# Kernel tuning notes

Hardware: AMD Instinct MI355X
Metric: run time of the kernel (lower is better)

## Reference

```python
import jax, jax.numpy as jnp
import numpy as np

N, E, DIN, DOUT, H = 100000, 1600000, 128, 128, 4
DH = DOUT // H
EPS = 1e-9


def setup_inputs() -> dict:
    key = jax.random.key(0)
    ks = jax.random.split(key, 16)
    g = lambda k, shape, fan: (jax.random.uniform(k, shape, jnp.float32, -1.0, 1.0)
                               * np.sqrt(6.0 / fan)).astype(jnp.float32)
    return {
        "vecs": jax.random.normal(ks[0], (N, DIN), jnp.float32),
        "adj_vals": jax.random.uniform(ks[1], (E,), jnp.float32),
        "W0": g(ks[2], (DIN, DOUT), DIN + DOUT),
        "b0": jnp.zeros((DOUT,), jnp.float32),
        "W1": g(ks[3], (H, DIN, DH), DIN + DH),          # per-head order1 weights
        "b1": jnp.zeros((H, DH), jnp.float32),
        "att0": g(ks[4], (H, DH), 1 + DH),               # attention_0_h{k}
        "att1": g(ks[5], (H, DH), 1 + DH),               # attention_1_h{k}
        "att_b0": jnp.zeros((H,), jnp.float32),
        "att_b1": jnp.zeros((H,), jnp.float32),
        "off0": jnp.zeros((1, DOUT), jnp.float32),
        "sc0": jnp.ones((1, DOUT), jnp.float32),
        "off1": jnp.zeros((1, DOUT), jnp.float32),
        "sc1": jnp.ones((1, DOUT), jnp.float32),
        "adj_rows": jax.random.randint(ks[6], (E,), 0, N, jnp.int32),
        "adj_cols": jax.random.randint(ks[7], (E,), 0, N, jnp.int32),
    }


def _row_norm(x, offset, scale):
    # tf.nn.moments over axis=1 + batch_normalization (per-row "norm" bias)
    mean = jnp.mean(x, axis=1, keepdims=True)
    var = jnp.mean(jnp.square(x - mean), axis=1, keepdims=True)
    return scale * (x - mean) * jax.lax.rsqrt(var + EPS) + offset


def reference(vecs, adj_vals, W0, b0, W1, b1, att0, att1, att_b0, att_b1,
              off0, sc0, off1, sc1, adj_rows, adj_cols):
    # ----- order-0 (self) path -----
    ret_self = jax.nn.relu(vecs @ W0 + b0)                      # [N, DOUT]
    ret_self = _row_norm(ret_self, off0, sc0)

    # ----- order-1 (neighbor) path, all heads at once -----
    vw = jnp.einsum('nd,hdk->hnk', vecs, W1)                    # [H, N, DH]
    a_self = jnp.einsum('hnk,hk->hn', vw, att0) + att_b0[:, None]   # [H, N]
    a_neigh = jnp.einsum('hnk,hk->hn', vw, att1) + att_b1[:, None]  # [H, N]

    # per-edge attention: relu(a1[col] + a2[row]); reweight sparse adj values
    alpha = jax.nn.relu(a_neigh[:, adj_cols] + a_self[:, adj_rows])  # [H, E]
    w = adj_vals[None, :] * alpha                                    # [H, E]

    # sparse-dense matmul: scatter-add weighted neighbor features to rows
    msg = w[:, :, None] * vw[:, adj_cols, :]                         # [H, E, DH]
    agg = jax.vmap(lambda m: jax.ops.segment_sum(m, adj_rows, num_segments=N))(msg)  # [H, N, DH]

    # subgraph (training) path: act(spmm) + bias (bias OUTSIDE the relu)
    ret_neigh = jax.nn.relu(agg) + b1[:, None, :]                    # [H, N, DH]
    ret_neigh = jnp.transpose(ret_neigh, (1, 0, 2)).reshape(N, DOUT)  # concat heads
    ret_neigh = _row_norm(ret_neigh, off1, sc1)

    # aggr == 'mean'
    return ret_neigh + ret_self
```

## Files before the change

kernel.cpp:

```cpp
#include <hip/hip_runtime.h>

#define N_NODES 100000
#define N_EDGES 1600000
#define DIN 128
#define DOUT 128
#define NH 4
#define DH 32
#define EPS 1e-9f

#define NBUK 256
#define NBUK_USED 196
#define CBLK 784
#define EPB  2048
#define COLMASK 0x1FFFF

typedef short bf16x8 __attribute__((ext_vector_type(8)));
typedef float f32x4 __attribute__((ext_vector_type(4)));

__device__ inline unsigned short f2bf(float x) {
    unsigned u = __float_as_uint(x);
    unsigned r = (u + 0x7fffu + ((u >> 16) & 1u)) >> 16;
    return (unsigned short)r;
}
__device__ inline float bflo(unsigned v) { return __uint_as_float(v << 16); }
__device__ inline float bfhi(unsigned v) { return __uint_as_float(v & 0xffff0000u); }

__global__ void k_cast(const float* __restrict__ in, unsigned short* __restrict__ out) {
    int t = blockIdx.x * 256 + threadIdx.x;
    const float4* p = (const float4*)(in + (size_t)t * 8);
    float4 a = p[0], b = p[1];
    unsigned short o[8] = {f2bf(a.x), f2bf(a.y), f2bf(a.z), f2bf(a.w),
                           f2bf(b.x), f2bf(b.y), f2bf(b.z), f2bf(b.w)};
    *(bf16x8*)(out + (size_t)t * 8) = *(bf16x8*)o;
}

__global__ void k_build_wtb(const float* __restrict__ W0, const float* __restrict__ W1,
                            unsigned short* __restrict__ Wtb) {
    int idx = blockIdx.x * 256 + threadIdx.x;
    int j = idx >> 7;
    int k = idx & 127;
    float v;
    if (j < 128) v = W0[k * 128 + j];
    else {
        int f = j - 128;
        v = W1[(f >> 5) * (DIN * DH) + k * DH + (f & 31)];
    }
    Wtb[j * 128 + k] = f2bf(v);
}

__global__ __launch_bounds__(256)
void k_gemm(const unsigned short* __restrict__ A, const unsigned short* __restrict__ B,
            const float* __restrict__ b0, float* __restrict__ comb_self,
            unsigned short* __restrict__ vwb) {
    __shared__ short As[64][136];
    __shared__ short Bs[128][136];
    int tid = threadIdx.x;
    int wave = tid >> 6;
    int lane = tid & 63;
    int m0 = blockIdx.y * 64;
    int j0 = blockIdx.x * 128;

    #pragma unroll
    for (int it = 0; it < 4; it++) {
        int ch = tid + it * 256;
        int row = ch >> 4, k8 = (ch & 15) << 3;
        *(bf16x8*)&As[row][k8] = *(const bf16x8*)&A[(size_t)(m0 + row) * 128 + k8];
    }
    #pragma unroll
    for (int it = 0; it < 8; it++) {
        int ch = tid + it * 256;
        int j = ch >> 4, k8 = (ch & 15) << 3;
        *(bf16x8*)&Bs[j][k8] = *(const bf16x8*)&B[(size_t)(j0 + j) * 128 + k8];
    }
    __syncthreads();

    int lrow = lane & 15;
    int g8 = (lane >> 4) << 3;
    f32x4 acc[4][2] = {};
    #pragma unroll
    for (int kk = 0; kk < 4; kk++) {
        int kb = kk * 32 + g8;
        bf16x8 a[4], b[2];
        #pragma unroll
        for (int r = 0; r < 4; r++) a[r] = *(bf16x8*)&As[r * 16 + lrow][kb];
        #pragma unroll
        for (int q = 0; q < 2; q++) b[q] = *(bf16x8*)&Bs[wave * 32 + q * 16 + lrow][kb];
        #pragma unroll
        for (int r = 0; r < 4; r++)
            #pragma unroll
            for (int q = 0; q < 2; q++)
                acc[r][q] = __builtin_amdgcn_mfma_f32_16x16x32_bf16(a[r], b[q], acc[r][q], 0, 0, 0);
    }

    int rbase = (lane >> 4) << 2;
    #pragma unroll
    for (int r = 0; r < 4; r++) {
        #pragma unroll
        for (int q = 0; q < 2; q++) {
            int gcol = j0 + wave * 32 + q * 16 + lrow;
            #pragma unroll
            for (int reg = 0; reg < 4; reg++) {
                int grow = m0 + r * 16 + rbase + reg;
                if (grow >= N_NODES) continue;
                float v = acc[r][q][reg];
                if (gcol < 128) {
                    comb_self[(size_t)grow * 128 + gcol] = fmaxf(v + b0[gcol], 0.f);
                } else {
                    vwb[(size_t)grow * 128 + (gcol - 128)] = f2bf(v);
                }
            }
        }
    }
}

__global__ void k_att(const unsigned short* __restrict__ vwb, const float* __restrict__ att0,
                      const float* __restrict__ att1, const float* __restrict__ attb0,
                      const float* __restrict__ attb1,
                      float* __restrict__ a_self, float* __restrict__ a_neigh) {
    int idx = blockIdx.x * 256 + threadIdx.x;
    if (idx >= N_NODES * NH) return;
    int n = idx >> 2;
    int h = idx & 3;
    const unsigned* vw = (const unsigned*)&vwb[(size_t)n * 128 + h * 32];
    const float* w0 = &att0[h * DH];
    const float* w1 = &att1[h * DH];
    float s0 = 0.f, s1 = 0.f;
    #pragma unroll
    for (int k = 0; k < 16; k++) {
        unsigned v = vw[k];
        float v0 = bflo(v), v1 = bfhi(v);
        s0 += v0 * w0[2 * k] + v1 * w0[2 * k + 1];
        s1 += v0 * w1[2 * k] + v1 * w1[2 * k + 1];
    }
    a_self[idx]  = s0 + attb0[h];
    a_neigh[idx] = s1 + attb1[h];
}


__global__ __launch_bounds__(256)
void k_bh(const int* __restrict__ rows, int* __restrict__ H) {
    __shared__ int h[NBUK];
    int t = threadIdx.x, b = blockIdx.x;
    h[t] = 0;
    __syncthreads();
    int e0 = b * EPB;
    int lim = min(EPB, N_EDGES - e0);
    for (int i = t; i < lim; i += 256)
        atomicAdd(&h[rows[e0 + i] >> 9], 1);
    __syncthreads();
    H[b * NBUK + t] = h[t];
}

__global__ __launch_bounds__(1024)
void k_bs(const int* __restrict__ H, int* __restrict__ BS, int* __restrict__ total) {
    __shared__ int sh[1024];
    int t = threadIdx.x, bk = blockIdx.x;
    int v = (t < CBLK) ? H[t * NBUK + bk] : 0;
    sh[t] = v;
    __syncthreads();
    for (int d = 1; d < 1024; d <<= 1) {
        int x = (t >= d) ? sh[t - d] : 0;
        __syncthreads();
        sh[t] += x;
        __syncthreads();
    }
    if (t < CBLK) BS[bk * CBLK + t] = sh[t] - v;
    if (t == 1023) total[bk] = sh[1023];
}

__global__ __launch_bounds__(256)
void k_ts(const int* __restrict__ total, int* __restrict__ bb, int* __restrict__ offs) {
    __shared__ int sh[256];
    int t = threadIdx.x;
    int v = total[t];
    sh[t] = v;
    __syncthreads();
    for (int d = 1; d < 256; d <<= 1) {
        int x = (t >= d) ? sh[t - d] : 0;
        __syncthreads();
        sh[t] += x;
        __syncthreads();
    }
    bb[t] = sh[t] - v;
    if (t == 255) { bb[256] = sh[255]; offs[N_NODES] = sh[255]; }
}

__global__ __launch_bounds__(256)
void k_cscat(const int* __restrict__ rows, const int* __restrict__ cols,
             const float* __restrict__ vals, const int* __restrict__ bb,
             const int* __restrict__ BS, int2* __restrict__ T) {
    __shared__ int cur[NBUK];
    int t = threadIdx.x, b = blockIdx.x;
    cur[t] = 0;
    __syncthreads();
    int e0 = b * EPB;
    int lim = min(EPB, N_EDGES - e0);
    for (int i = t; i < lim; i += 256) {
        int e = e0 + i;
        int r = rows[e];
        int bk = r >> 9;
        int rank = atomicAdd(&cur[bk], 1);
        int dest = bb[bk] + BS[bk * CBLK + b] + rank;
        int2 p;
        p.x = cols[e] | ((r & 511) << 17);
        p.y = __float_as_int(vals[e]);
        T[dest] = p;
    }
}

__global__ __launch_bounds__(512)
void k_fine(const int2* __restrict__ T, const int* __restrict__ bb,
            int* __restrict__ offs, int2* __restrict__ cav) {
    __shared__ int cnt[512], rb[512], cur[512], wsum[8];
    int t = threadIdx.x, b = blockIdx.x;
    int base = bb[b];
    int m = bb[b + 1] - base;
    cnt[t] = 0;
    cur[t] = 0;
    __syncthreads();
    for (int i = t; i < m; i += 512)
        atomicAdd(&cnt[(T[base + i].x >> 17) & 511], 1);
    __syncthreads();
    int lane = t & 63, w = t >> 6;
    int v = cnt[t];
    int incl = v;
    #pragma unroll
    for (int d = 1; d < 64; d <<= 1) {
        int x = __shfl_up(incl, d, 64);
        if (lane >= d) incl += x;
    }
    if (lane == 63) wsum[w] = incl;
    __syncthreads();
    int wb = 0;
    #pragma unroll
    for (int i = 0; i < 8; i++) if (i < w) wb += wsum[i];
    rb[t] = incl - v + wb;
    int rg = b * 512 + t;
    if (rg < N_NODES) offs[rg] = base + rb[t];
    __syncthreads();
    for (int i = t; i < m; i += 512) {
        int2 p = T[base + i];
        int r = (p.x >> 17) & 511;
        int k = atomicAdd(&cur[r], 1);
        cav[base + rb[r] + k] = p;
    }
}

__global__ __launch_bounds__(256)
void k_final(const float* __restrict__ comb_self, const unsigned short* __restrict__ vwb,
             const int2* __restrict__ cav, const float* __restrict__ a_self,
             const float* __restrict__ a_neigh,
             const int* __restrict__ offs, const float* __restrict__ b1,
             const float* __restrict__ off0, const float* __restrict__ sc0,
             const float* __restrict__ off1, const float* __restrict__ sc1,
             float* __restrict__ out) {
    int wave = threadIdx.x >> 6;
    int lane = threadIdx.x & 63;
    int n = blockIdx.x * 4 + wave;
    if (n >= N_NODES) return;
    int h = lane >> 4;
    int f0 = lane * 2;
    int f1 = f0 + 1;

    float as_ = a_self[n * 4 + h];
    int lo = offs[n], hi = offs[n + 1];
    float acc0 = 0.f, acc1 = 0.f;

#define BODY(I) { \
        int2 p_ = cav[(I)]; \
        int c_ = p_.x & COLMASK; \
        float av_ = __int_as_float(p_.y); \
        float an_ = a_neigh[c_ * 4 + h]; \
        unsigned v_ = *(const unsigned*)&vwb[(size_t)c_ * 128 + f0]; \
        float al_ = fmaxf(an_ + as_, 0.f) * av_; \
        acc0 += al_ * bflo(v_); \
        acc1 += al_ * bfhi(v_); }

    int i = lo;
    for (; i + 4 <= hi; i += 4) { BODY(i) BODY(i + 1) BODY(i + 2) BODY(i + 3) }
    for (; i < hi; i++) BODY(i)
#undef BODY

    float x0 = fmaxf(acc0, 0.f) + b1[f0];
    float x1 = fmaxf(acc1, 0.f) + b1[f1];
    float s = x0 + x1;
    #pragma unroll
    for (int d = 32; d > 0; d >>= 1) s += __shfl_xor(s, d, 64);
    float mean = s * (1.f / 128.f);
    float d0 = x0 - mean, d1 = x1 - mean;
    float q = d0 * d0 + d1 * d1;
    #pragma unroll
    for (int d = 32; d > 0; d >>= 1) q += __shfl_xor(q, d, 64);
    float rinv = rsqrtf(q * (1.f / 128.f) + EPS);
    float y0 = sc1[f0] * d0 * rinv + off1[f0];
    float y1 = sc1[f1] * d1 * rinv + off1[f1];

    float2 u = *(const float2*)&comb_self[(size_t)n * 128 + f0];
    float s2 = u.x + u.y;
    #pragma unroll
    for (int d = 32; d > 0; d >>= 1) s2 += __shfl_xor(s2, d, 64);
    float m2 = s2 * (1.f / 128.f);
    float e0 = u.x - m2, e1 = u.y - m2;
    float q2 = e0 * e0 + e1 * e1;
    #pragma unroll
    for (int d = 32; d > 0; d >>= 1) q2 += __shfl_xor(q2, d, 64);
    float rinv2 = rsqrtf(q2 * (1.f / 128.f) + EPS);
    float z0 = sc0[f0] * e0 * rinv2 + off0[f0];
    float z1 = sc0[f1] * e1 * rinv2 + off0[f1];

    *(float2*)&out[(size_t)n * 128 + f0] = make_float2(y0 + z0, y1 + z1);
}

extern "C" void kernel_launch(void* const* d_in, const int* in_sizes, int n_in,
                              void* d_out, int out_size, void* d_ws, size_t ws_size,
                              hipStream_t stream) {
    const float* vecs     = (const float*)d_in[0];
    const float* adj_vals = (const float*)d_in[1];
    const float* W0       = (const float*)d_in[2];
    const float* b0       = (const float*)d_in[3];
    const float* W1       = (const float*)d_in[4];
    const float* b1       = (const float*)d_in[5];
    const float* att0     = (const float*)d_in[6];
    const float* att1     = (const float*)d_in[7];
    const float* att_b0   = (const float*)d_in[8];
    const float* att_b1   = (const float*)d_in[9];
    const float* off0     = (const float*)d_in[10];
    const float* sc0      = (const float*)d_in[11];
    const float* off1     = (const float*)d_in[12];
    const float* sc1      = (const float*)d_in[13];
    const int*   adj_rows = (const int*)d_in[14];
    const int*   adj_cols = (const int*)d_in[15];
    float* out = (float*)d_out;

    char* ws = (char*)d_ws;
    size_t o = 0;
    auto alloc = [&](size_t bytes) {
        char* p = ws + o;
        o += (bytes + 255) & ~(size_t)255;
        return p;
    };
    const int MPAD = 100032;
    unsigned short* vecsb = (unsigned short*)alloc((size_t)MPAD * 128 * 2);
    unsigned short* Wtb   = (unsigned short*)alloc((size_t)256 * 128 * 2);
    float* comb_self      = (float*)alloc((size_t)N_NODES * 128 * 4);
    unsigned short* vwb   = (unsigned short*)alloc((size_t)N_NODES * 128 * 2);
    float* a_self         = (float*)alloc((size_t)N_NODES * NH * 4);
    float* a_neigh        = (float*)alloc((size_t)N_NODES * NH * 4);
    int*   offs           = (int*)alloc((size_t)(N_NODES + 1) * 4);
    int*   H              = (int*)alloc((size_t)CBLK * NBUK * 4);
    int*   BS             = (int*)alloc((size_t)NBUK * CBLK * 4);
    int*   total          = (int*)alloc((size_t)NBUK * 4);
    int*   bb             = (int*)alloc((size_t)(NBUK + 1) * 4);
    int2*  T              = (int2*)vecsb;
    int2*  cav            = (int2*)(vecsb + (size_t)N_EDGES * 4);

    k_cast<<<(N_NODES * 128 / 8 + 255) / 256, 256, 0, stream>>>(vecs, vecsb);
    k_build_wtb<<<128, 256, 0, stream>>>(W0, W1, Wtb);

    dim3 g2(2, MPAD / 64);
    k_gemm<<<g2, 256, 0, stream>>>(vecsb, Wtb, b0, comb_self, vwb);

    k_att<<<(N_NODES * NH + 255) / 256, 256, 0, stream>>>(vwb, att0, att1, att_b0, att_b1,
                                                          a_self, a_neigh);

    k_bh<<<CBLK, 256, 0, stream>>>(adj_rows, H);
    k_bs<<<NBUK, 1024, 0, stream>>>(H, BS, total);
    k_ts<<<1, 256, 0, stream>>>(total, bb, offs);
    k_cscat<<<CBLK, 256, 0, stream>>>(adj_rows, adj_cols, adj_vals, bb, BS, T);
    k_fine<<<NBUK_USED, 512, 0, stream>>>(T, bb, offs, cav);

    k_final<<<(N_NODES + 3) / 4, 256, 0, stream>>>(comb_self, vwb, cav, a_self, a_neigh,
                                                   offs, b1, off0, sc0, off1, sc1, out);
}
```

Before: 353.8 us.

## Fuse bf16 cast and attention logits into GEMM, store self path in bf16

The separate fp32→bf16 cast kernel is removed. The GEMM now loads fp32 vecs directly and converts them while staging into shared memory. The attention dot products are computed in the GEMM epilogue from the accumulators using lane shuffles, which removes the k_att kernel and its re-read of vw. The self-path activations are stored as bf16 instead of fp32, halving that write and the later read in k_final, at some precision cost before the row normalisation. Edge scratch buffers get their own workspace allocations instead of aliasing the removed cast buffer.

```diff
diff --git a/kernel.cpp b/kernel.cpp
--- a/kernel.cpp
+++ b/kernel.cpp
@@ -24,15 +24,6 @@
 }
 __device__ inline float bflo(unsigned v) { return __uint_as_float(v << 16); }
 __device__ inline float bfhi(unsigned v) { return __uint_as_float(v & 0xffff0000u); }
-
-__global__ void k_cast(const float* __restrict__ in, unsigned short* __restrict__ out) {
-    int t = blockIdx.x * 256 + threadIdx.x;
-    const float4* p = (const float4*)(in + (size_t)t * 8);
-    float4 a = p[0], b = p[1];
-    unsigned short o[8] = {f2bf(a.x), f2bf(a.y), f2bf(a.z), f2bf(a.w),
-                           f2bf(b.x), f2bf(b.y), f2bf(b.z), f2bf(b.w)};
-    *(bf16x8*)(out + (size_t)t * 8) = *(bf16x8*)o;
-}
 
 __global__ void k_build_wtb(const float* __restrict__ W0, const float* __restrict__ W1,
                             unsigned short* __restrict__ Wtb) {
@@ -49,9 +40,12 @@
 }
 
 __global__ __launch_bounds__(256)
-void k_gemm(const unsigned short* __restrict__ A, const unsigned short* __restrict__ B,
-            const float* __restrict__ b0, float* __restrict__ comb_self,
-            unsigned short* __restrict__ vwb) {
+void k_gemm(const float* __restrict__ A, const unsigned short* __restrict__ B,
+            const float* __restrict__ b0,
+            const float* __restrict__ att0, const float* __restrict__ att1,
+            const float* __restrict__ attb0, const float* __restrict__ attb1,
+            unsigned short* __restrict__ comb_selfb, unsigned short* __restrict__ vwb,
+            float* __restrict__ a_self, float* __restrict__ a_neigh) {
     __shared__ short As[64][136];
     __shared__ short Bs[128][136];
     int tid = threadIdx.x;
@@ -64,7 +58,16 @@
     for (int it = 0; it < 4; it++) {
         int ch = tid + it * 256;
         int row = ch >> 4, k8 = (ch & 15) << 3;
-        *(bf16x8*)&As[row][k8] = *(const bf16x8*)&A[(size_t)(m0 + row) * 128 + k8];
+        int gr = m0 + row;
+        float4 lo = make_float4(0.f, 0.f, 0.f, 0.f), hi = lo;
+        if (gr < N_NODES) {
+            const float* src = &A[(size_t)gr * 128 + k8];
+            lo = *(const float4*)src;
+            hi = *(const float4*)(src + 4);
+        }
+        unsigned short o[8] = {f2bf(lo.x), f2bf(lo.y), f2bf(lo.z), f2bf(lo.w),
+                               f2bf(hi.x), f2bf(hi.y), f2bf(hi.z), f2bf(hi.w)};
+        *(bf16x8*)&As[row][k8] = *(bf16x8*)o;
     }
     #pragma unroll
     for (int it = 0; it < 8; it++) {
@@ -104,36 +107,43 @@
                 if (grow >= N_NODES) continue;
                 float v = acc[r][q][reg];
                 if (gcol < 128) {
-                    comb_self[(size_t)grow * 128 + gcol] = fmaxf(v + b0[gcol], 0.f);
+                    comb_selfb[(size_t)grow * 128 + gcol] = f2bf(fmaxf(v + b0[gcol], 0.f));
                 } else {
                     vwb[(size_t)grow * 128 + (gcol - 128)] = f2bf(v);
                 }
             }
         }
     }
-}
-
-__global__ void k_att(const unsigned short* __restrict__ vwb, const float* __restrict__ att0,
-                      const float* __restrict__ att1, const float* __restrict__ attb0,
-                      const float* __restrict__ attb1,
-                      float* __restrict__ a_self, float* __restrict__ a_neigh) {
-    int idx = blockIdx.x * 256 + threadIdx.x;
-    if (idx >= N_NODES * NH) return;
-    int n = idx >> 2;
-    int h = idx & 3;
-    const unsigned* vw = (const unsigned*)&vwb[(size_t)n * 128 + h * 32];
-    const float* w0 = &att0[h * DH];
-    const float* w1 = &att1[h * DH];
-    float s0 = 0.f, s1 = 0.f;
-    #pragma unroll
-    for (int k = 0; k < 16; k++) {
-        unsigned v = vw[k];
-        float v0 = bflo(v), v1 = bfhi(v);
-        s0 += v0 * w0[2 * k] + v1 * w0[2 * k + 1];
-        s1 += v0 * w1[2 * k] + v1 * w1[2 * k + 1];
-    }
-    a_self[idx]  = s0 + attb0[h];
-    a_neigh[idx] = s1 + attb1[h];
+
+    if (j0 == 128) {
+        float w0q0 = att0[wave * 32 + lrow],      w0q1 = att0[wave * 32 + 16 + lrow];
+        float w1q0 = att1[wave * 32 + lrow],      w1q1 = att1[wave * 32 + 16 + lrow];
+        float ab0 = attb0[wave], ab1 = attb1[wave];
+        #pragma unroll
+        for (int r = 0; r < 4; r++) {
+            float t0[4], t1[4];
+            #pragma unroll
+            for (int reg = 0; reg < 4; reg++) {
+                t0[reg] = acc[r][0][reg] * w0q0 + acc[r][1][reg] * w0q1;
+                t1[reg] = acc[r][0][reg] * w1q0 + acc[r][1][reg] * w1q1;
+                #pragma unroll
+                for (int d = 1; d < 16; d <<= 1) {
+                    t0[reg] += __shfl_xor(t0[reg], d, 64);
+                    t1[reg] += __shfl_xor(t1[reg], d, 64);
+                }
+            }
+            if (lrow == 0) {
+                #pragma unroll
+                for (int reg = 0; reg < 4; reg++) {
+                    int grow = m0 + r * 16 + rbase + reg;
+                    if (grow < N_NODES) {
+                        a_self[grow * 4 + wave]  = t0[reg] + ab0;
+                        a_neigh[grow * 4 + wave] = t1[reg] + ab1;
+                    }
+                }
+            }
+        }
+    }
 }
 
 
@@ -247,7 +257,8 @@
 }
 
 __global__ __launch_bounds__(256)
-void k_final(const float* __restrict__ comb_self, const unsigned short* __restrict__ vwb,
+void k_final(const unsigned short* __restrict__ comb_selfb,
+             const unsigned short* __restrict__ vwb,
              const int2* __restrict__ cav, const float* __restrict__ a_self,
              const float* __restrict__ a_neigh,
              const int* __restrict__ offs, const float* __restrict__ b1,
@@ -295,12 +306,13 @@
     float y0 = sc1[f0] * d0 * rinv + off1[f0];
     float y1 = sc1[f1] * d1 * rinv + off1[f1];
 
-    float2 u = *(const float2*)&comb_self[(size_t)n * 128 + f0];
-    float s2 = u.x + u.y;
+    unsigned uu = *(const unsigned*)&comb_selfb[(size_t)n * 128 + f0];
+    float ux = bflo(uu), uy = bfhi(uu);
+    float s2 = ux + uy;
     #pragma unroll
     for (int d = 32; d > 0; d >>= 1) s2 += __shfl_xor(s2, d, 64);
     float m2 = s2 * (1.f / 128.f);
-    float e0 = u.x - m2, e1 = u.y - m2;
+    float e0 = ux - m2, e1 = uy - m2;
     float q2 = e0 * e0 + e1 * e1;
     #pragma unroll
     for (int d = 32; d > 0; d >>= 1) q2 += __shfl_xor(q2, d, 64);
@@ -340,9 +352,8 @@
         return p;
     };
     const int MPAD = 100032;
-    unsigned short* vecsb = (unsigned short*)alloc((size_t)MPAD * 128 * 2);
     unsigned short* Wtb   = (unsigned short*)alloc((size_t)256 * 128 * 2);
-    float* comb_self      = (float*)alloc((size_t)N_NODES * 128 * 4);
+    unsigned short* comb_selfb = (unsigned short*)alloc((size_t)N_NODES * 128 * 2);
     unsigned short* vwb   = (unsigned short*)alloc((size_t)N_NODES * 128 * 2);
     float* a_self         = (float*)alloc((size_t)N_NODES * NH * 4);
     float* a_neigh        = (float*)alloc((size_t)N_NODES * NH * 4);
@@ -351,17 +362,14 @@
     int*   BS             = (int*)alloc((size_t)NBUK * CBLK * 4);
     int*   total          = (int*)alloc((size_t)NBUK * 4);
     int*   bb             = (int*)alloc((size_t)(NBUK + 1) * 4);
-    int2*  T              = (int2*)vecsb;
-    int2*  cav            = (int2*)(vecsb + (size_t)N_EDGES * 4);
-
-    k_cast<<<(N_NODES * 128 / 8 + 255) / 256, 256, 0, stream>>>(vecs, vecsb);
+    int2*  T              = (int2*)alloc((size_t)N_EDGES * 8);
+    int2*  cav            = (int2*)alloc((size_t)N_EDGES * 8);
+
     k_build_wtb<<<128, 256, 0, stream>>>(W0, W1, Wtb);
 
     dim3 g2(2, MPAD / 64);
-    k_gemm<<<g2, 256, 0, stream>>>(vecsb, Wtb, b0, comb_self, vwb);
-
-    k_att<<<(N_NODES * NH + 255) / 256, 256, 0, stream>>>(vwb, att0, att1, att_b0, att_b1,
-                                                          a_self, a_neigh);
+    k_gemm<<<g2, 256, 0, stream>>>(vecs, Wtb, b0, att0, att1, att_b0, att_b1,
+                                   comb_selfb, vwb, a_self, a_neigh);
 
     k_bh<<<CBLK, 256, 0, stream>>>(adj_rows, H);
     k_bs<<<NBUK, 1024, 0, stream>>>(H, BS, total);
@@ -369,6 +377,6 @@
     k_cscat<<<CBLK, 256, 0, stream>>>(adj_rows, adj_cols, adj_vals, bb, BS, T);
     k_fine<<<NBUK_USED, 512, 0, stream>>>(T, bb, offs, cav);
 
-    k_final<<<(N_NODES + 3) / 4, 256, 0, stream>>>(comb_self, vwb, cav, a_self, a_neigh,
+    k_final<<<(N_NODES + 3) / 4, 256, 0, stream>>>(comb_selfb, vwb, cav, a_self, a_neigh,
                                                    offs, b1, off0, sc0, off1, sc1, out);
 }
```

Measured after the change: 338.3 us. 1.05x faster.
